# Kernel optimization log

Hardware: AMD Instinct MI355X
Metric: run time of the kernel (lower is better)

The kernel has to match this reference:

```python
import jax, jax.numpy as jnp
import numpy as np

N_NODES = 50000
N_EDGES = 800000
N_GRAPHS = 64
IN_DIM = 768
HID = 256
OUT_DIM = 4
N_REL = 3
N_LAYERS = 3


def setup_inputs() -> dict:
    key = jax.random.key(0)
    ks = jax.random.split(key, 20)
    inp = {
        "x": jax.random.normal(ks[0], (N_NODES, IN_DIM), dtype=jnp.float32),
        "edge_index": jax.random.randint(ks[1], (2, N_EDGES), 0, N_NODES, dtype=jnp.int32),
        "edge_type": jax.random.randint(ks[2], (N_EDGES,), 0, N_REL, dtype=jnp.int32),
        "batch": jnp.sort(jax.random.randint(ks[3], (N_NODES,), 0, N_GRAPHS, dtype=jnp.int32)),
        # input projection
        "in_w": jax.random.normal(ks[4], (IN_DIM, HID), dtype=jnp.float32) * (IN_DIM ** -0.5),
        "in_b": jnp.zeros((HID,), dtype=jnp.float32),
        # RGCN layers (stacked over num_layers)
        "root_w": jax.random.normal(ks[5], (N_LAYERS, HID, HID), dtype=jnp.float32) * (HID ** -0.5),
        "rel_w": jax.random.normal(ks[6], (N_LAYERS, N_REL, HID, HID), dtype=jnp.float32) * (HID ** -0.5),
        "conv_b": jnp.zeros((N_LAYERS, HID), dtype=jnp.float32),
        "ln_w": jnp.ones((N_LAYERS, HID), dtype=jnp.float32),
        "ln_b": jnp.zeros((N_LAYERS, HID), dtype=jnp.float32),
        # classifier MLP
        "cls_w1": jax.random.normal(ks[7], (HID, HID), dtype=jnp.float32) * (HID ** -0.5),
        "cls_b1": jnp.zeros((HID,), dtype=jnp.float32),
        "cls_w2": jax.random.normal(ks[8], (HID, OUT_DIM), dtype=jnp.float32) * (HID ** -0.5),
        "cls_b2": jnp.zeros((OUT_DIM,), dtype=jnp.float32),
    }
    return inp


def _rgcn_conv(h, src, dst, edge_type, root, rel, bias):
    # PyG RGCNConv (default aggr='mean'): out = h @ root + sum_r mean_dst(h[src] | type==r) @ W_r + b
    n = h.shape[0]
    out = h @ root + bias
    for r in range(N_REL):
        m = (edge_type == r).astype(h.dtype)  # [E]
        msg = h[src] * m[:, None]             # gather + mask
        s = jax.ops.segment_sum(msg, dst, num_segments=n)   # [N, HID]
        cnt = jax.ops.segment_sum(m, dst, num_segments=n)   # [N]
        mean = s / jnp.maximum(cnt, 1.0)[:, None]
        out = out + mean @ rel[r]
    return out


def _layer_norm(h, w, b, eps=1e-5):
    mu = jnp.mean(h, axis=-1, keepdims=True)
    var = jnp.mean((h - mu) ** 2, axis=-1, keepdims=True)
    return (h - mu) * jax.lax.rsqrt(var + eps) * w + b


def reference(x, edge_index, edge_type, batch, in_w, in_b, root_w, rel_w, conv_b,
              ln_w, ln_b, cls_w1, cls_b1, cls_w2, cls_b2):
    src, dst = edge_index[0], edge_index[1]
    h = x @ in_w + in_b
    for i in range(N_LAYERS):
        h_new = _rgcn_conv(h, src, dst, edge_type, root_w[i], rel_w[i], conv_b[i])
        h = h_new + h  # residual (shapes always equal: HID->HID)
        h = jax.nn.relu(h)
        h = _layer_norm(h, ln_w[i], ln_b[i])
        # dropout is identity in eval mode
    # global max pool over each graph
    g = jax.ops.segment_max(h, batch, num_segments=N_GRAPHS)  # [B, HID]
    z = jax.nn.relu(g @ cls_w1 + cls_b1)
    return z @ cls_w2 + cls_b2
```

## Files before the change

kernel.cpp:

```cpp
#include <hip/hip_runtime.h>
#include <cstdint>
#include <cstddef>

#define NN 50000
#define NE 800000
#define NG 64
#define IND 768
#define HID 256
#define NREL 3
#define NLAY 3

typedef __attribute__((ext_vector_type(4))) float f32x4;
typedef __attribute__((ext_vector_type(8))) short s16x8;

__global__ void k_zero_int(int* __restrict__ p, int n) {
  int i = blockIdx.x * 256 + threadIdx.x;
  if (i < n) p[i] = 0;
}

__global__ void k_hist(const int* __restrict__ dst, int* __restrict__ deg) {
  int e = blockIdx.x * 256 + threadIdx.x;
  if (e < NE) atomicAdd(&deg[dst[e]], 1);
}

__global__ __launch_bounds__(1024) void k_scan(const int* __restrict__ deg,
                                               int* __restrict__ row_start,
                                               int* __restrict__ cursor) {
  __shared__ int wsum[16];
  int t = threadIdx.x;
  int lane = t & 63, wid = t >> 6;
  int running = 0;
  if (t == 0) row_start[0] = 0;
  for (int base = 0; base < NN; base += 4096) {
    int idx = base + t * 4;
    int4 d = *(const int4*)(deg + idx);
    int s = d.x + d.y + d.z + d.w;
    int sc = s;
    #pragma unroll
    for (int off = 1; off < 64; off <<= 1) {
      int o = __shfl_up(sc, off);
      if (lane >= off) sc += o;
    }
    if (lane == 63) wsum[wid] = sc;
    __syncthreads();
    if (t == 0) {
      int a = 0;
      #pragma unroll
      for (int i = 0; i < 16; ++i) { a += wsum[i]; wsum[i] = a; }
    }
    __syncthreads();
    int woff = (wid == 0) ? 0 : wsum[wid - 1];
    int excl = running + woff + (sc - s);
    int e0 = excl, e1 = e0 + d.x, e2 = e1 + d.y, e3 = e2 + d.z, e4 = e3 + d.w;
    if (idx     < NN) { cursor[idx]     = e0; row_start[idx + 1] = e1; }
    if (idx + 1 < NN) { cursor[idx + 1] = e1; row_start[idx + 2] = e2; }
    if (idx + 2 < NN) { cursor[idx + 2] = e2; row_start[idx + 3] = e3; }
    if (idx + 3 < NN) { cursor[idx + 3] = e3; row_start[idx + 4] = e4; }
    running += wsum[15];
    __syncthreads();
  }
}

__global__ void k_scatter(const int* __restrict__ src, const int* __restrict__ dst,
                          const int* __restrict__ ety, int* __restrict__ cursor,
                          unsigned* __restrict__ csr) {
  int e = blockIdx.x * 256 + threadIdx.x;
  if (e >= NE) return;
  int pos = atomicAdd(&cursor[dst[e]], 1);
  csr[pos] = (unsigned)src[e] | ((unsigned)ety[e] << 16);
}

__global__ void k_graph_bounds(const int* __restrict__ batch, int* __restrict__ gstart) {
  int i = blockIdx.x * 256 + threadIdx.x;
  if (i >= NN) return;
  int b = batch[i];
  int bp = (i == 0) ? -1 : batch[i - 1];
  for (int g = bp + 1; g <= b; ++g) gstart[g] = i;
  if (i == NN - 1) {
    for (int g = b + 1; g <= NG; ++g) gstart[g] = NN;
  }
}

__global__ __launch_bounds__(64) void k_aggregate(const float* __restrict__ h,
                                                  const int* __restrict__ row_start,
                                                  const unsigned* __restrict__ csr,
                                                  float* __restrict__ agg) {
  int n = blockIdx.x;
  int t = threadIdx.x;
  int s = row_start[n], e = row_start[n + 1];
  float4 a0 = {0, 0, 0, 0}, a1 = {0, 0, 0, 0}, a2 = {0, 0, 0, 0};
  int c0 = 0, c1 = 0, c2 = 0;
  __shared__ unsigned buf[64];
  for (int base = s; base < e; base += 64) {
    int m = e - base; if (m > 64) m = 64;
    __syncthreads();
    if (t < m) buf[t] = csr[base + t];
    __syncthreads();
    for (int j = 0; j < m; ++j) {
      unsigned p = buf[j];
      int src = p & 0xFFFF;
      int ty = (int)(p >> 16);
      float4 v = *(const float4*)(h + (size_t)src * HID + t * 4);
      if (ty == 0)      { a0.x += v.x; a0.y += v.y; a0.z += v.z; a0.w += v.w; c0++; }
      else if (ty == 1) { a1.x += v.x; a1.y += v.y; a1.z += v.z; a1.w += v.w; c1++; }
      else              { a2.x += v.x; a2.y += v.y; a2.z += v.z; a2.w += v.w; c2++; }
    }
  }
  float i0 = 1.f / (float)(c0 > 1 ? c0 : 1);
  float i1 = 1.f / (float)(c1 > 1 ? c1 : 1);
  float i2 = 1.f / (float)(c2 > 1 ? c2 : 1);
  float* o = agg + (size_t)n * (NREL * HID) + t * 4;
  float4 r0 = {a0.x * i0, a0.y * i0, a0.z * i0, a0.w * i0};
  float4 r1 = {a1.x * i1, a1.y * i1, a1.z * i1, a1.w * i1};
  float4 r2 = {a2.x * i2, a2.y * i2, a2.z * i2, a2.w * i2};
  *(float4*)(o)           = r0;
  *(float4*)(o + HID)     = r1;
  *(float4*)(o + 2 * HID) = r2;
}

__device__ __forceinline__ unsigned short bf16rne(float f) {
  union { float f; unsigned u; } x; x.f = f;
  unsigned r = (x.u + 0x7FFFu + ((x.u >> 16) & 1u)) >> 16;
  return (unsigned short)r;
}
__device__ __forceinline__ float bf2f(unsigned short h) {
  union { unsigned u; float f; } x; x.u = ((unsigned)h) << 16;
  return x.f;
}

__global__ void k_cvt(const float* __restrict__ s1, int K1e,
                      const float* __restrict__ s2, int Ktot,
                      unsigned short* __restrict__ hi, unsigned short* __restrict__ lo) {
  int t = blockIdx.x * 256 + threadIdx.x;
  if (t >= Ktot * 256) return;
  int c = t & 255, k = t >> 8;
  float v = (k < K1e) ? s1[(size_t)k * 256 + c] : s2[(size_t)(k - K1e) * 256 + c];
  unsigned short h = bf16rne(v);
  unsigned short l = bf16rne(v - bf2f(h));
  size_t o = ((size_t)(k >> 3) * 256 + c) * 8 + (k & 7);
  hi[o] = h; lo[o] = l;
}

__device__ __forceinline__ void load_lds16b(const void* g, void* l) {
  __builtin_amdgcn_global_load_lds(
      (const __attribute__((address_space(1))) unsigned*)g,
      (__attribute__((address_space(3))) unsigned*)l, 16, 0, 0);
}

template <int EPI>
__global__ __launch_bounds__(256, 1) void k_gemm_mfma(
    const float* __restrict__ A1, int lda1,
    const float* __restrict__ A2, int lda2, int K1,
    const unsigned short* __restrict__ Bhi, const unsigned short* __restrict__ Blo,
    const float* __restrict__ bias, const float* __restrict__ res,
    const float* __restrict__ lnw, const float* __restrict__ lnb,
    float* __restrict__ C, int M, int K) {
  __shared__ __align__(16) unsigned short AsH[4 * 64 * 8], AsL[4 * 64 * 8];
  __shared__ __align__(16) unsigned short BsH[4 * 256 * 8], BsL[4 * 256 * 8];
  __shared__ float lnred[64 * 4 * 2];
  int tid = (int)threadIdx.x;
  int lane = tid & 63, wv = tid >> 6;
  int n0 = (int)blockIdx.x * 64;
  int srow = tid >> 2, sg = tid & 3;
  int grow = n0 + srow; if (grow > M - 1) grow = M - 1;
  int c16 = lane & 15, kg = lane >> 4;
  int col0 = wv * 64;

  f32x4 acc[4][4] = {};

  for (int kt = 0; kt < K / 32; ++kt) {
    int kk = kt * 32;
    const float* Ap; int ld, kc;
    if (kk < K1) { Ap = A1; ld = lda1; kc = kk; }
    else         { Ap = A2; ld = lda2; kc = kk - K1; }
    const float* ap = Ap + (size_t)grow * ld + kc + sg * 8;
    float4 a0 = *(const float4*)ap;
    float4 a1 = *(const float4*)(ap + 4);
    __syncthreads();
    #pragma unroll
    for (int i = 0; i < 8; ++i) {
      int id = wv * 8 + i;
      const unsigned short* src = (id < 16) ? Bhi : Blo;
      unsigned short* dst = (id < 16) ? BsH : BsL;
      int rem = id & 15, g = rem >> 2, ch = rem & 3;
      load_lds16b(src + (size_t)(kt * 4 + g) * 2048 + (ch * 64 + lane) * 8,
                  dst + (g * 256 + ch * 64) * 8);
    }
    float va[8] = {a0.x, a0.y, a0.z, a0.w, a1.x, a1.y, a1.z, a1.w};
    s16x8 hv, lv;
    #pragma unroll
    for (int j = 0; j < 8; ++j) {
      unsigned short h = bf16rne(va[j]);
      hv[j] = (short)h;
      lv[j] = (short)bf16rne(va[j] - bf2f(h));
    }
    *(s16x8*)&AsH[(sg * 64 + srow) * 8] = hv;
    *(s16x8*)&AsL[(sg * 64 + srow) * 8] = lv;
    __syncthreads();
    s16x8 ah[4], al[4];
    #pragma unroll
    for (int ri = 0; ri < 4; ++ri) {
      int ao = (kg * 64 + ri * 16 + c16) * 8;
      ah[ri] = *(const s16x8*)&AsH[ao];
      al[ri] = *(const s16x8*)&AsL[ao];
    }
    #pragma unroll
    for (int ci = 0; ci < 4; ++ci) {
      int bo = (kg * 256 + col0 + ci * 16 + c16) * 8;
      s16x8 bh = *(const s16x8*)&BsH[bo];
      s16x8 bl = *(const s16x8*)&BsL[bo];
      #pragma unroll
      for (int ri = 0; ri < 4; ++ri) {
        acc[ri][ci] = __builtin_amdgcn_mfma_f32_16x16x32_bf16(ah[ri], bh, acc[ri][ci], 0, 0, 0);
        acc[ri][ci] = __builtin_amdgcn_mfma_f32_16x16x32_bf16(ah[ri], bl, acc[ri][ci], 0, 0, 0);
        acc[ri][ci] = __builtin_amdgcn_mfma_f32_16x16x32_bf16(al[ri], bh, acc[ri][ci], 0, 0, 0);
      }
    }
  }

  float bw[4], lw[4], lb[4];
  #pragma unroll
  for (int ci = 0; ci < 4; ++ci) {
    int col = col0 + ci * 16 + c16;
    bw[ci] = bias[col];
    if (EPI == 1) { lw[ci] = lnw[col]; lb[ci] = lnb[col]; }
  }
  if (EPI == 0) {
    #pragma unroll
    for (int ri = 0; ri < 4; ++ri)
      #pragma unroll
      for (int q = 0; q < 4; ++q) {
        int row = n0 + ri * 16 + kg * 4 + q;
        if (row < M) {
          #pragma unroll
          for (int ci = 0; ci < 4; ++ci)
            C[(size_t)row * 256 + col0 + ci * 16 + c16] = acc[ri][ci][q] + bw[ci];
        }
      }
  } else {
    #pragma unroll
    for (int ri = 0; ri < 4; ++ri)
      #pragma unroll
      for (int q = 0; q < 4; ++q) {
        int rl = ri * 16 + kg * 4 + q;
        int rr = n0 + rl; int rc = rr < M ? rr : M - 1;
        float s = 0.f, s2 = 0.f;
        #pragma unroll
        for (int ci = 0; ci < 4; ++ci) {
          float r = res[(size_t)rc * 256 + col0 + ci * 16 + c16];
          float v = fmaxf(acc[ri][ci][q] + bw[ci] + r, 0.f);
          acc[ri][ci][q] = v;
          s += v; s2 += v * v;
        }
        #pragma unroll
        for (int m = 1; m < 16; m <<= 1) {
          s  += __shfl_xor(s, m);
          s2 += __shfl_xor(s2, m);
        }
        if (c16 == 0) {
          lnred[(rl * 4 + wv) * 2]     = s;
          lnred[(rl * 4 + wv) * 2 + 1] = s2;
        }
      }
    __syncthreads();
    #pragma unroll
    for (int ri = 0; ri < 4; ++ri)
      #pragma unroll
      for (int q = 0; q < 4; ++q) {
        int rl = ri * 16 + kg * 4 + q;
        float S = 0.f, S2 = 0.f;
        #pragma unroll
        for (int w = 0; w < 4; ++w) {
          S  += lnred[(rl * 4 + w) * 2];
          S2 += lnred[(rl * 4 + w) * 2 + 1];
        }
        float mean = S * (1.f / 256.f);
        float var = S2 * (1.f / 256.f) - mean * mean;
        float rstd = rsqrtf(var + 1e-5f);
        int row = n0 + rl;
        if (row < M) {
          #pragma unroll
          for (int ci = 0; ci < 4; ++ci)
            C[(size_t)row * 256 + col0 + ci * 16 + c16] =
                (acc[ri][ci][q] - mean) * rstd * lw[ci] + lb[ci];
        }
      }
  }
}

__global__ void k_pool(const float* __restrict__ h, const int* __restrict__ gstart,
                       float* __restrict__ g) {
  int gi = blockIdx.x;
  int c = blockIdx.y * 128 + threadIdx.x;
  int s = gstart[gi], e = gstart[gi + 1];
  float m = -3.402823466e+38f;
  for (int n = s; n < e; ++n) m = fmaxf(m, h[(size_t)n * HID + c]);
  g[gi * HID + c] = m;
}

__global__ __launch_bounds__(256) void k_classifier(const float* __restrict__ g,
                                                    const float* __restrict__ w1,
                                                    const float* __restrict__ b1,
                                                    const float* __restrict__ w2,
                                                    const float* __restrict__ b2,
                                                    float* __restrict__ out) {
  int gi = blockIdx.x, t = (int)threadIdx.x;
  __shared__ float gs[HID], zs[HID];
  gs[t] = g[gi * HID + t];
  __syncthreads();
  float s = b1[t];
  for (int k = 0; k < HID; ++k) s = fmaf(gs[k], w1[k * HID + t], s);
  zs[t] = fmaxf(s, 0.f);
  __syncthreads();
  if (t < 4) {
    float o = b2[t];
    for (int k = 0; k < HID; ++k) o = fmaf(zs[k], w2[k * 4 + t], o);
    out[gi * 4 + t] = o;
  }
}

extern "C" void kernel_launch(void* const* d_in, const int* in_sizes, int n_in,
                              void* d_out, int out_size, void* d_ws, size_t ws_size,
                              hipStream_t stream) {
  const float* x      = (const float*)d_in[0];
  const int*   eidx   = (const int*)d_in[1];
  const int*   etype  = (const int*)d_in[2];
  const int*   batch  = (const int*)d_in[3];
  const float* in_w   = (const float*)d_in[4];
  const float* in_b   = (const float*)d_in[5];
  const float* root_w = (const float*)d_in[6];
  const float* rel_w  = (const float*)d_in[7];
  const float* conv_b = (const float*)d_in[8];
  const float* ln_w   = (const float*)d_in[9];
  const float* ln_b   = (const float*)d_in[10];
  const float* cls_w1 = (const float*)d_in[11];
  const float* cls_b1 = (const float*)d_in[12];
  const float* cls_w2 = (const float*)d_in[13];
  const float* cls_b2 = (const float*)d_in[14];
  float* out = (float*)d_out;

  char* ws = (char*)d_ws;
  size_t off = 0;
  auto alloc = [&](size_t bytes) -> void* {
    void* p = ws + off;
    off += (bytes + 255) & ~(size_t)255;
    return p;
  };
  float*    bufA      = (float*)alloc(sizeof(float) * (size_t)NN * HID);
  float*    bufB      = (float*)alloc(sizeof(float) * (size_t)NN * HID);
  float*    agg       = (float*)alloc(sizeof(float) * (size_t)NN * NREL * HID);
  unsigned* csr       = (unsigned*)alloc(sizeof(unsigned) * NE);
  int*      deg       = (int*)alloc(sizeof(int) * 53248);
  int*      row_start = (int*)alloc(sizeof(int) * (NN + 1));
  int*      cursor    = (int*)alloc(sizeof(int) * NN);
  int*      gstart    = (int*)alloc(sizeof(int) * (NG + 1));
  float*    gpool     = (float*)alloc(sizeof(float) * NG * HID);
  unsigned short* wInH = (unsigned short*)alloc(sizeof(unsigned short) * 96 * 256 * 8);
  unsigned short* wInL = (unsigned short*)alloc(sizeof(unsigned short) * 96 * 256 * 8);
  unsigned short* wLH[NLAY];
  unsigned short* wLL[NLAY];
  for (int L = 0; L < NLAY; ++L) {
    wLH[L] = (unsigned short*)alloc(sizeof(unsigned short) * 128 * 256 * 8);
    wLL[L] = (unsigned short*)alloc(sizeof(unsigned short) * 128 * 256 * 8);
  }
  (void)ws_size; (void)in_sizes; (void)n_in; (void)out_size;

  const int* esrc = eidx;
  const int* edst = eidx + NE;

  k_cvt<<<IND, 256, 0, stream>>>(in_w, IND, nullptr, IND, wInH, wInL);
  for (int L = 0; L < NLAY; ++L)
    k_cvt<<<HID + NREL * HID, 256, 0, stream>>>(
        root_w + (size_t)L * HID * HID, HID,
        rel_w + (size_t)L * NREL * HID * HID, HID + NREL * HID, wLH[L], wLL[L]);

  k_zero_int<<<(53248 + 255) / 256, 256, 0, stream>>>(deg, 53248);
  k_hist<<<(NE + 255) / 256, 256, 0, stream>>>(edst, deg);
  k_scan<<<1, 1024, 0, stream>>>(deg, row_start, cursor);
  k_scatter<<<(NE + 255) / 256, 256, 0, stream>>>(esrc, edst, etype, cursor, csr);
  k_graph_bounds<<<(NN + 255) / 256, 256, 0, stream>>>(batch, gstart);

  int gemm_grid = (NN + 63) / 64;
  k_gemm_mfma<0><<<gemm_grid, 256, 0, stream>>>(
      x, IND, nullptr, 0, IND, wInH, wInL, in_b,
      nullptr, nullptr, nullptr, bufA, NN, IND);

  float* hcur = bufA;
  float* hnext = bufB;
  for (int L = 0; L < NLAY; ++L) {
    k_aggregate<<<NN, 64, 0, stream>>>(hcur, row_start, csr, agg);
    k_gemm_mfma<1><<<gemm_grid, 256, 0, stream>>>(
        hcur, HID, agg, NREL * HID, HID, wLH[L], wLL[L],
        conv_b + L * HID, hcur, ln_w + L * HID, ln_b + L * HID,
        hnext, NN, HID + NREL * HID);
    float* tmp = hcur; hcur = hnext; hnext = tmp;
  }

  k_pool<<<dim3(NG, 2), 128, 0, stream>>>(hcur, gstart, gpool);
  k_classifier<<<NG, 256, 0, stream>>>(gpool, cls_w1, cls_b1, cls_w2, cls_b2, out);
}
```

Measured before the change: 1.337 ms.

## Unroll gather loop, prefetch GEMM A tiles, swizzle LDS, split max-pool

The aggregation loop now issues four independent neighbour-row loads before accumulating, which raises memory-level parallelism. The MFMA GEMM loads the next K-tile of A into registers while the current tile is being multiplied, and applies an XOR swizzle to the A tile in LDS to reduce bank conflicts. The global max-pool is split into two kernels: eight partial chunks per graph, then a reduction. This raises parallelism from 128 blocks, at the cost of an extra launch and a scratch buffer.

```diff
diff --git a/kernel.cpp b/kernel.cpp
--- a/kernel.cpp
+++ b/kernel.cpp
@@ -91,19 +91,30 @@
   float4 a0 = {0, 0, 0, 0}, a1 = {0, 0, 0, 0}, a2 = {0, 0, 0, 0};
   int c0 = 0, c1 = 0, c2 = 0;
   __shared__ unsigned buf[64];
+  auto accum = [&](unsigned p, float4 v) {
+    int ty = (int)(p >> 16);
+    if (ty == 0)      { a0.x += v.x; a0.y += v.y; a0.z += v.z; a0.w += v.w; c0++; }
+    else if (ty == 1) { a1.x += v.x; a1.y += v.y; a1.z += v.z; a1.w += v.w; c1++; }
+    else              { a2.x += v.x; a2.y += v.y; a2.z += v.z; a2.w += v.w; c2++; }
+  };
   for (int base = s; base < e; base += 64) {
     int m = e - base; if (m > 64) m = 64;
     __syncthreads();
     if (t < m) buf[t] = csr[base + t];
     __syncthreads();
-    for (int j = 0; j < m; ++j) {
+    int j = 0;
+    for (; j + 4 <= m; j += 4) {
+      unsigned p0 = buf[j], p1 = buf[j + 1], p2 = buf[j + 2], p3 = buf[j + 3];
+      float4 v0 = *(const float4*)(h + (size_t)(p0 & 0xFFFF) * HID + t * 4);
+      float4 v1 = *(const float4*)(h + (size_t)(p1 & 0xFFFF) * HID + t * 4);
+      float4 v2 = *(const float4*)(h + (size_t)(p2 & 0xFFFF) * HID + t * 4);
+      float4 v3 = *(const float4*)(h + (size_t)(p3 & 0xFFFF) * HID + t * 4);
+      accum(p0, v0); accum(p1, v1); accum(p2, v2); accum(p3, v3);
+    }
+    for (; j < m; ++j) {
       unsigned p = buf[j];
-      int src = p & 0xFFFF;
-      int ty = (int)(p >> 16);
-      float4 v = *(const float4*)(h + (size_t)src * HID + t * 4);
-      if (ty == 0)      { a0.x += v.x; a0.y += v.y; a0.z += v.z; a0.w += v.w; c0++; }
-      else if (ty == 1) { a1.x += v.x; a1.y += v.y; a1.z += v.z; a1.w += v.w; c1++; }
-      else              { a2.x += v.x; a2.y += v.y; a2.z += v.z; a2.w += v.w; c2++; }
+      float4 v = *(const float4*)(h + (size_t)(p & 0xFFFF) * HID + t * 4);
+      accum(p, v);
     }
   }
   float i0 = 1.f / (float)(c0 > 1 ? c0 : 1);
@@ -167,42 +178,55 @@
   int col0 = wv * 64;
 
   f32x4 acc[4][4] = {};
-
-  for (int kt = 0; kt < K / 32; ++kt) {
-    int kk = kt * 32;
-    const float* Ap; int ld, kc;
-    if (kk < K1) { Ap = A1; ld = lda1; kc = kk; }
-    else         { Ap = A2; ld = lda2; kc = kk - K1; }
-    const float* ap = Ap + (size_t)grow * ld + kc + sg * 8;
-    float4 a0 = *(const float4*)ap;
-    float4 a1 = *(const float4*)(ap + 4);
+  int nkt = K / 32;
+
+  float4 a0, a1;
+  {
+    const float* ap = A1 + (size_t)grow * lda1 + sg * 8;
+    a0 = *(const float4*)ap;
+    a1 = *(const float4*)(ap + 4);
+  }
+
+  for (int kt = 0; kt < nkt; ++kt) {
     __syncthreads();
     #pragma unroll
     for (int i = 0; i < 8; ++i) {
       int id = wv * 8 + i;
-      const unsigned short* src = (id < 16) ? Bhi : Blo;
-      unsigned short* dst = (id < 16) ? BsH : BsL;
+      const unsigned short* srcp = (id < 16) ? Bhi : Blo;
+      unsigned short* dstp = (id < 16) ? BsH : BsL;
       int rem = id & 15, g = rem >> 2, ch = rem & 3;
-      load_lds16b(src + (size_t)(kt * 4 + g) * 2048 + (ch * 64 + lane) * 8,
-                  dst + (g * 256 + ch * 64) * 8);
-    }
-    float va[8] = {a0.x, a0.y, a0.z, a0.w, a1.x, a1.y, a1.z, a1.w};
-    s16x8 hv, lv;
-    #pragma unroll
-    for (int j = 0; j < 8; ++j) {
-      unsigned short h = bf16rne(va[j]);
-      hv[j] = (short)h;
-      lv[j] = (short)bf16rne(va[j] - bf2f(h));
-    }
-    *(s16x8*)&AsH[(sg * 64 + srow) * 8] = hv;
-    *(s16x8*)&AsL[(sg * 64 + srow) * 8] = lv;
+      load_lds16b(srcp + (size_t)(kt * 4 + g) * 2048 + (ch * 64 + lane) * 8,
+                  dstp + (g * 256 + ch * 64) * 8);
+    }
+    {
+      float va[8] = {a0.x, a0.y, a0.z, a0.w, a1.x, a1.y, a1.z, a1.w};
+      s16x8 hv, lv;
+      #pragma unroll
+      for (int j = 0; j < 8; ++j) {
+        unsigned short h = bf16rne(va[j]);
+        hv[j] = (short)h;
+        lv[j] = (short)bf16rne(va[j] - bf2f(h));
+      }
+      int aoff = (sg * 64 + (srow ^ (sg << 2))) * 8;
+      *(s16x8*)&AsH[aoff] = hv;
+      *(s16x8*)&AsL[aoff] = lv;
+    }
     __syncthreads();
     s16x8 ah[4], al[4];
     #pragma unroll
     for (int ri = 0; ri < 4; ++ri) {
-      int ao = (kg * 64 + ri * 16 + c16) * 8;
+      int ao = (kg * 64 + ((ri * 16 + c16) ^ (kg << 2))) * 8;
       ah[ri] = *(const s16x8*)&AsH[ao];
       al[ri] = *(const s16x8*)&AsL[ao];
+    }
+    int kn = (kt + 1) * 32;
+    if (kn < K) {
+      const float* Ap; int ld, kc;
+      if (kn < K1) { Ap = A1; ld = lda1; kc = kn; }
+      else         { Ap = A2; ld = lda2; kc = kn - K1; }
+      const float* ap = Ap + (size_t)grow * ld + kc + sg * 8;
+      a0 = *(const float4*)ap;
+      a1 = *(const float4*)(ap + 4);
     }
     #pragma unroll
     for (int ci = 0; ci < 4; ++ci) {
@@ -288,13 +312,31 @@
   }
 }
 
-__global__ void k_pool(const float* __restrict__ h, const int* __restrict__ gstart,
-                       float* __restrict__ g) {
-  int gi = blockIdx.x;
-  int c = blockIdx.y * 128 + threadIdx.x;
-  int s = gstart[gi], e = gstart[gi + 1];
+__global__ __launch_bounds__(256) void k_pool1(const float* __restrict__ h,
+                                               const int* __restrict__ gstart,
+                                               float* __restrict__ part) {
+  int gi = blockIdx.x, ck = blockIdx.y;
+  int c = (int)threadIdx.x;
+  int s = gstart[gi], e = gstart[gi + 1], len = e - s;
+  int cs = s + (int)(((long long)len * ck) >> 3);
+  int ce = s + (int)(((long long)len * (ck + 1)) >> 3);
   float m = -3.402823466e+38f;
-  for (int n = s; n < e; ++n) m = fmaxf(m, h[(size_t)n * HID + c]);
+  int n = cs;
+  for (; n + 2 <= ce; n += 2) {
+    float x0 = h[(size_t)n * HID + c];
+    float x1 = h[(size_t)(n + 1) * HID + c];
+    m = fmaxf(m, fmaxf(x0, x1));
+  }
+  if (n < ce) m = fmaxf(m, h[(size_t)n * HID + c]);
+  part[((size_t)gi * 8 + ck) * HID + c] = m;
+}
+
+__global__ __launch_bounds__(256) void k_pool2(const float* __restrict__ part,
+                                               float* __restrict__ g) {
+  int gi = blockIdx.x, c = (int)threadIdx.x;
+  float m = part[((size_t)gi * 8) * HID + c];
+  #pragma unroll
+  for (int k = 1; k < 8; ++k) m = fmaxf(m, part[((size_t)gi * 8 + k) * HID + c]);
   g[gi * HID + c] = m;
 }
 
@@ -355,6 +397,7 @@
   int*      cursor    = (int*)alloc(sizeof(int) * NN);
   int*      gstart    = (int*)alloc(sizeof(int) * (NG + 1));
   float*    gpool     = (float*)alloc(sizeof(float) * NG * HID);
+  float*    gpart     = (float*)alloc(sizeof(float) * NG * 8 * HID);
   unsigned short* wInH = (unsigned short*)alloc(sizeof(unsigned short) * 96 * 256 * 8);
   unsigned short* wInL = (unsigned short*)alloc(sizeof(unsigned short) * 96 * 256 * 8);
   unsigned short* wLH[NLAY];
@@ -396,6 +439,7 @@
     float* tmp = hcur; hcur = hnext; hnext = tmp;
   }
 
-  k_pool<<<dim3(NG, 2), 128, 0, stream>>>(hcur, gstart, gpool);
+  k_pool1<<<dim3(NG, 8), 256, 0, stream>>>(hcur, gstart, gpart);
+  k_pool2<<<NG, 256, 0, stream>>>(gpart, gpool);
   k_classifier<<<NG, 256, 0, stream>>>(gpool, cls_w1, cls_b1, cls_w2, cls_b2, out);
 }
```

Result: slower. 1.559 ms (+16.6%).
